# Optimization experiments

Hardware: AMD Instinct MI355X
Metric: run time of the kernel (lower is better)

Reference implementation:

```python
import jax, jax.numpy as jnp
import numpy as np
import math

DIM = 2048; H = 16; QR = 1536; KVR = 512; DN = 128; DR = 64; DV = 128
BS = 4; S = 1024
QK_HEAD = DN + DR  # 192


def _rms(x, w, eps=1e-6):
    v = jnp.mean(x * x, axis=-1, keepdims=True)
    return w * (x * jax.lax.rsqrt(v + eps))


def _rope_cos_sin(seq_len, dim):
    inv_freq = 1.0 / (10000.0 ** (jnp.arange(0, dim, 2, dtype=jnp.float32) / dim))
    t = jnp.arange(seq_len, dtype=jnp.float32)
    freqs = jnp.einsum('s,d->sd', t, inv_freq)
    freqs = jnp.concatenate([freqs, freqs], axis=-1)  # [S, dim]
    return jnp.cos(freqs), jnp.sin(freqs)


def _rotate_half(x):
    x1, x2 = jnp.split(x, 2, axis=-1)
    return jnp.concatenate([-x2, x1], axis=-1)


def setup_inputs() -> dict:
    key = jax.random.key(0)
    ks = jax.random.split(key, 12)
    sd = 0.02
    x = jax.random.normal(ks[0], (BS, S, DIM), dtype=jnp.float32)
    # causal additive mask [b, s, t]
    i = jnp.arange(S)
    causal = jnp.where(i[:, None] >= i[None, :], 0.0, -1e9).astype(jnp.float32)
    mask = jnp.broadcast_to(causal, (BS, S, S))
    return {
        'x': x,
        'mask': mask,
        'wq_a_w': jax.random.normal(ks[1], (QR, DIM)) * sd,
        'wq_a_b': jnp.zeros((QR,), jnp.float32),
        'q_norm_w': jnp.ones((QR,), jnp.float32),
        'wq_b_w': jax.random.normal(ks[2], (H * QK_HEAD, QR)) * sd,
        'wq_b_b': jnp.zeros((H * QK_HEAD,), jnp.float32),
        'wkv_a_w': jax.random.normal(ks[3], (KVR + DR, DIM)) * sd,
        'wkv_a_b': jnp.zeros((KVR + DR,), jnp.float32),
        'kv_norm_w': jnp.ones((KVR,), jnp.float32),
        'wkv_b_w': jax.random.normal(ks[4], (H * (DN + DV), KVR)) * sd,
        'wo_w': jax.random.normal(ks[5], (DIM, H * DV)) * sd,
        'wo_b': jnp.zeros((DIM,), jnp.float32),
    }


def reference(x, mask, wq_a_w, wq_a_b, q_norm_w, wq_b_w, wq_b_b,
              wkv_a_w, wkv_a_b, kv_norm_w, wkv_b_w, wo_w, wo_b):
    bs, seq_len, _ = x.shape
    # Q low-rank path
    q = x @ wq_a_w.T + wq_a_b                     # [b,s,QR]
    q = _rms(q, q_norm_w)
    q = q @ wq_b_w.T + wq_b_b                     # [b,s,H*192]
    q = q.reshape(bs, seq_len, H, QK_HEAD)
    q_nope, q_pe = q[..., :DN], q[..., DN:]       # [b,s,h,128], [b,s,h,64]
    # compressed KV path
    kv = x @ wkv_a_w.T + wkv_a_b                  # [b,s,KVR+64]
    c, k_pe = kv[..., :KVR], kv[..., KVR:]        # [b,s,512], [b,s,64]
    # RoPE on the rope sub-dims
    cos, sin = _rope_cos_sin(seq_len, DR)         # [s,64]
    cos4 = cos[None, :, None, :]
    sin4 = sin[None, :, None, :]
    q_pe = q_pe * cos4 + _rotate_half(q_pe) * sin4
    k_pe4 = k_pe[:, :, None, :]
    k_pe = (k_pe4 * cos4 + _rotate_half(k_pe4) * sin4)[:, :, 0, :]  # [b,s,64]
    # weight absorption: wkv_b viewed [H, DN+DV, KVR]
    wkv_b = wkv_b_w.reshape(H, DN + DV, KVR)
    q_abs = jnp.einsum('bshd,hdc->bshc', q_nope, wkv_b[:, :DN])      # [b,s,h,512]
    c_n = _rms(c, kv_norm_w)                                         # [b,t,512]
    scores = (jnp.einsum('bshc,btc->bsht', q_abs, c_n)
              + jnp.einsum('bshr,btr->bsht', q_pe, k_pe)) / math.sqrt(QK_HEAD)
    scores = scores + mask[:, :, None, :]
    scores = jax.nn.softmax(scores, axis=-1)
    o = jnp.einsum('bsht,btc->bshc', scores, c_n)                    # [b,s,h,512]
    o = jnp.einsum('bshc,hdc->bshd', o, wkv_b[:, -DV:])              # [b,s,h,128]
    o = o.reshape(bs, seq_len, H * DV)
    return o @ wo_w.T + wo_b
```

## Files before the change

### kernel.cpp

```cpp
#include <hip/hip_runtime.h>


typedef __attribute__((ext_vector_type(8))) short bf16x8;
typedef __attribute__((ext_vector_type(4))) float f32x4;
typedef __attribute__((ext_vector_type(4))) int i32x4;
typedef unsigned short ushort_t;
typedef unsigned int uint32;

typedef const __attribute__((address_space(1))) void* gas_ptr;
typedef __attribute__((address_space(3))) void* las_ptr;

#define DEV __device__ __forceinline__
#define WAITVM(N) asm volatile("s_waitcnt vmcnt(" #N ")" ::: "memory")
#define WAITLGKM0 asm volatile("s_waitcnt lgkmcnt(0)" ::: "memory")

DEV float b2f(ushort_t u) { return __uint_as_float(((uint32)u) << 16); }
DEV ushort_t f2b(float f) {
  uint32 u = __float_as_uint(f);
  return (ushort_t)((u + 0x7fffu + ((u >> 16) & 1u)) >> 16);
}
DEV uint32 pkb(float lo, float hi) { return (uint32)f2b(lo) | ((uint32)f2b(hi) << 16); }

DEV void c4seg(const float4* __restrict__ in, ushort4* __restrict__ out, int i, int n4) {
  if (i < n4) {
    float4 v = in[i];
    ushort4 o; o.x = f2b(v.x); o.y = f2b(v.y); o.z = f2b(v.z); o.w = f2b(v.w);
    out[i] = o;
  }
}
DEV void vbseg(const float* __restrict__ in, ushort_t* __restrict__ out, int i4, int dofs) {
  int c4 = i4 & 127, d = (i4 >> 7) & 127, h = i4 >> 14;
  const float4 v = *(const float4*)(in + ((long)(h * 256 + dofs + d)) * 512 + c4 * 4);
  ushort4 o; o.x = f2b(v.x); o.y = f2b(v.y); o.z = f2b(v.z); o.w = f2b(v.w);
  ((ushort4*)out)[i4] = o;
}
__global__ __launch_bounds__(256) void castall_k(
    const float* __restrict__ x, const float* __restrict__ wq_a_w,
    const float* __restrict__ wkv_a_w, const float* __restrict__ wq_b_w,
    const float* __restrict__ wo_w, const float* __restrict__ wkv_b_w,
    ushort_t* __restrict__ xb, ushort_t* __restrict__ wcomb,
    ushort_t* __restrict__ wqb, ushort_t* __restrict__ wo,
    ushort_t* __restrict__ wkvbv, ushort_t* __restrict__ wkvbn) {
  int blk = blockIdx.x, tid = threadIdx.x;
  if (blk < 8192) {
    c4seg((const float4*)x, (ushort4*)xb, blk * 256 + tid, 2097152);
  } else if (blk < 11264) {
    c4seg((const float4*)wq_a_w, (ushort4*)wcomb, (blk - 8192) * 256 + tid, 786432);
  } else if (blk < 12416) {
    c4seg((const float4*)wkv_a_w, (ushort4*)(wcomb + 1536 * 2048),
          (blk - 11264) * 256 + tid, 294912);
  } else if (blk < 17024) {
    c4seg((const float4*)wq_b_w, (ushort4*)wqb, (blk - 12416) * 256 + tid, 1179648);
  } else if (blk < 21120) {
    c4seg((const float4*)wo_w, (ushort4*)wo, (blk - 17024) * 256 + tid, 1048576);
  } else if (blk < 22144) {
    vbseg(wkv_b_w, wkvbv, (blk - 21120) * 256 + tid, 128);
  } else {
    vbseg(wkv_b_w, wkvbn, (blk - 22144) * 256 + tid, 0);
  }
}

__global__ __launch_bounds__(512) void rmskv_k(const float* __restrict__ qa_in,
                                               ushort_t* __restrict__ qan,
                                               const float* __restrict__ q_norm_w,
                                               const float* __restrict__ kvf,
                                               const float* __restrict__ kv_norm_w,
                                               ushort_t* __restrict__ kcat,
                                               ushort_t* __restrict__ vtp,
                                               ushort_t* __restrict__ kabs) {
  __shared__ float sbuf[8];
  __shared__ ushort_t sh[8 * 512];
  int blk = blockIdx.x, tid = threadIdx.x;
  int wv = tid >> 6, lane = tid & 63;
  if (blk < 4096) {
    long row = blk;
    const float* p = qa_in + row * 1536;
    float v0 = p[tid], v1 = p[tid + 512], v2 = p[tid + 1024];
    float ss = v0 * v0 + v1 * v1 + v2 * v2;
#pragma unroll
    for (int d = 1; d <= 32; d <<= 1) ss += __shfl_xor(ss, d);
    if (lane == 0) sbuf[wv] = ss;
    __syncthreads();
    float tot = 0.f;
#pragma unroll
    for (int i = 0; i < 8; ++i) tot += sbuf[i];
    float sc = rsqrtf(tot * (1.0f / 1536.0f) + 1e-6f);
    qan[row * 1536 + tid] = f2b(v0 * sc * q_norm_w[tid]);
    qan[row * 1536 + tid + 512] = f2b(v1 * sc * q_norm_w[tid + 512]);
    qan[row * 1536 + tid + 1024] = f2b(v2 * sc * q_norm_w[tid + 1024]);
  } else {
    int kb = blk - 4096;
    long row = (long)kb * 8 + wv;
    const float* p = kvf + row * 576;
    float4 v0 = *(const float4*)(p + lane * 8);
    float4 v1 = *(const float4*)(p + lane * 8 + 4);
    float ss = v0.x * v0.x + v0.y * v0.y + v0.z * v0.z + v0.w * v0.w
             + v1.x * v1.x + v1.y * v1.y + v1.z * v1.z + v1.w * v1.w;
#pragma unroll
    for (int d = 1; d <= 32; d <<= 1) ss += __shfl_xor(ss, d);
    float sc = rsqrtf(ss * (1.0f / 512.0f) + 1e-6f);
    float4 w0 = *(const float4*)(kv_norm_w + lane * 8);
    float4 w1 = *(const float4*)(kv_norm_w + lane * 8 + 4);
    ushort_t tmp[8];
    tmp[0] = f2b(v0.x * sc * w0.x); tmp[1] = f2b(v0.y * sc * w0.y);
    tmp[2] = f2b(v0.z * sc * w0.z); tmp[3] = f2b(v0.w * sc * w0.w);
    tmp[4] = f2b(v1.x * sc * w1.x); tmp[5] = f2b(v1.y * sc * w1.y);
    tmp[6] = f2b(v1.z * sc * w1.z); tmp[7] = f2b(v1.w * sc * w1.w);
    *(uint4*)(kcat + row * 576 + lane * 8) = *(uint4*)tmp;
    *(uint4*)(sh + wv * 512 + lane * 8) = *(uint4*)tmp;
    if (lane < 32) {
      int t = (int)(row & 1023);
      float x1 = p[512 + lane], x2 = p[544 + lane];
      float ang = (float)t * powf(10000.0f, -(float)lane * (1.0f / 32.0f));
      float s, c; sincosf(ang, &s, &c);
      ushort_t r1 = f2b(x1 * c - x2 * s), r2 = f2b(x2 * c + x1 * s);
      kcat[row * 576 + 512 + lane] = r1;
      kcat[row * 576 + 544 + lane] = r2;
#pragma unroll
      for (int h = 0; h < 16; ++h) {
        long base = ((long)h * 4096 + row) * 192;
        kabs[base + 128 + lane] = r1;
        kabs[base + 160 + lane] = r2;
      }
    }
    __syncthreads();
    ushort_t t8[8];
#pragma unroll
    for (int j = 0; j < 8; ++j) t8[j] = sh[j * 512 + tid];
    int b = kb >> 7, tb = kb & 127;
    *(uint4*)(vtp + (((long)b * 128 + tb) * 512 + tid) * 8) = *(uint4*)t8;
  }
}

template <bool OUT_BF16>
__global__ __launch_bounds__(256) void gemm_bt_k(
    const ushort_t* __restrict__ A, int lda, long sAz,
    const ushort_t* __restrict__ B, int ldb, long sBz,
    void* __restrict__ C, int ldc, long sCz,
    const float* __restrict__ bias, float scale,
    int M, int N, int K) {
  __shared__ ushort_t As[2 * 4096];
  __shared__ ushort_t Bs[2 * 4096];
  int tid = threadIdx.x;
  int wave = tid >> 6, lane = tid & 63;
  int row0 = blockIdx.x * 128, col0 = blockIdx.y * 128;
  int z = blockIdx.z;
  const ushort_t* Az = A + (long)z * sAz;
  const ushort_t* Bz = B + (long)z * sBz;
  int wr = wave >> 1, wc = wave & 1;
  int lr = lane & 15, kq = lane >> 4;

  f32x4 acc[4][4];
#pragma unroll
  for (int m = 0; m < 4; ++m)
#pragma unroll
    for (int n = 0; n < 4; ++n) acc[m][n] = (f32x4){0.f, 0.f, 0.f, 0.f};

  auto stage = [&](int buf, int k0) {
#pragma unroll
    for (int rnd = 0; rnd < 2; ++rnd) {
      int e = rnd * 2048 + wave * 512 + lane * 8;
      int tr = e >> 5, tc = e & 31;
      int ar = row0 + tr; if (ar >= M) ar = M - 1;
      int br = col0 + tr; if (br >= N) br = N - 1;
      __builtin_amdgcn_global_load_lds((gas_ptr)(Az + (long)ar * lda + (k0 + tc)),
          (las_ptr)(As + buf * 4096 + rnd * 2048 + wave * 512), 16, 0, 0);
      __builtin_amdgcn_global_load_lds((gas_ptr)(Bz + (long)br * ldb + (k0 + tc)),
          (las_ptr)(Bs + buf * 4096 + rnd * 2048 + wave * 512), 16, 0, 0);
    }
  };

  stage(0, 0);
  int nk = K >> 5;
  for (int kt = 0; kt < nk; ++kt) {
    int cur = kt & 1;
    if (kt + 1 < nk) { stage(cur ^ 1, (kt + 1) * 32); WAITVM(4); }
    else { WAITVM(0); }
    __builtin_amdgcn_s_barrier();
    __builtin_amdgcn_sched_barrier(0);
    const ushort_t* Ac = As + cur * 4096;
    const ushort_t* Bc = Bs + cur * 4096;
    bf16x8 a[4], bb[4];
#pragma unroll
    for (int m = 0; m < 4; ++m)
      a[m] = *(const bf16x8*)(Ac + (wr * 64 + m * 16 + lr) * 32 + kq * 8);
#pragma unroll
    for (int n = 0; n < 4; ++n)
      bb[n] = *(const bf16x8*)(Bc + (wc * 64 + n * 16 + lr) * 32 + kq * 8);
#pragma unroll
    for (int m = 0; m < 4; ++m)
#pragma unroll
      for (int n = 0; n < 4; ++n)
        acc[m][n] = __builtin_amdgcn_mfma_f32_16x16x32_bf16(bb[n], a[m], acc[m][n], 0, 0, 0);
    __builtin_amdgcn_s_barrier();
  }

#pragma unroll
  for (int m = 0; m < 4; ++m) {
    int gr = row0 + wr * 64 + m * 16 + lr;
    if (gr >= M) continue;
#pragma unroll
    for (int n = 0; n < 4; ++n) {
      int cb = col0 + wc * 64 + n * 16 + kq * 4;
      if (cb >= N) continue;
      f32x4 v = acc[m][n];
#pragma unroll
      for (int r = 0; r < 4; ++r) v[r] = v[r] * scale + (bias ? bias[cb + r] : 0.f);
      long ci = (long)z * sCz + (long)gr * ldc + cb;
      if constexpr (OUT_BF16) {
        ushort4 pk; pk.x = f2b(v[0]); pk.y = f2b(v[1]); pk.z = f2b(v[2]); pk.w = f2b(v[3]);
        *(ushort4*)((ushort_t*)C + ci) = pk;
      } else {
        *(f32x4*)((float*)C + ci) = v;
      }
    }
  }
}

template <int MODE>
__global__ __launch_bounds__(256) void gemm64_k(
    const ushort_t* __restrict__ A, int lda,
    const ushort_t* __restrict__ B, int ldb,
    void* __restrict__ C, int ldc,
    const float* __restrict__ bias,
    void* __restrict__ C2, const float* __restrict__ bias2,
    int M, int N, int K) {
  __shared__ ushort_t As[2 * 8192];
  __shared__ ushort_t Bs[2 * 8192];
  int tid = threadIdx.x;
  int wave = tid >> 6, lane = tid & 63;
  int bid = blockIdx.y * gridDim.x + blockIdx.x;
  int nwg = gridDim.x * gridDim.y;
  int swz = (bid & 7) * (nwg >> 3) + (bid >> 3);
  int bx = swz % gridDim.x, by = swz / gridDim.x;
  int row0 = bx * 128, col0 = by * 128;
  int wr = wave >> 1, wc = wave & 1;
  int lr = lane & 15, kq = lane >> 4;
  int rsw = lr & 7;

  f32x4 acc[4][4];
#pragma unroll
  for (int m = 0; m < 4; ++m)
#pragma unroll
    for (int n = 0; n < 4; ++n) acc[m][n] = (f32x4){0.f, 0.f, 0.f, 0.f};

  auto stage = [&](int buf, int k0) {
#pragma unroll
    for (int ii = 0; ii < 4; ++ii) {
      int e = ii * 256 + tid;
      int r = e >> 3, c = e & 7;
      int scol = ((c ^ (r & 7)) << 3);
      int ar = row0 + r; if (ar >= M) ar = M - 1;
      int br = col0 + r; if (br >= N) br = N - 1;
      __builtin_amdgcn_global_load_lds((gas_ptr)(A + (long)ar * lda + k0 + scol),
          (las_ptr)(As + buf * 8192 + e * 8), 16, 0, 0);
      __builtin_amdgcn_global_load_lds((gas_ptr)(B + (long)br * ldb + k0 + scol),
          (las_ptr)(Bs + buf * 8192 + e * 8), 16, 0, 0);
    }
  };

  stage(0, 0);
  int nk = K >> 6;
  for (int kt = 0; kt < nk; ++kt) {
    int cur = kt & 1;
    if (kt + 1 < nk) { stage(cur ^ 1, (kt + 1) * 64); WAITVM(8); }
    else { WAITVM(0); }
    __builtin_amdgcn_s_barrier();
    __builtin_amdgcn_sched_barrier(0);
    const ushort_t* Ac = As + cur * 8192;
    const ushort_t* Bc = Bs + cur * 8192;
#pragma unroll
    for (int ks = 0; ks < 2; ++ks) {
      bf16x8 a[4], bb[4];
#pragma unroll
      for (int m = 0; m < 4; ++m) {
        int row = wr * 64 + m * 16 + lr;
        a[m] = *(const bf16x8*)(Ac + row * 64 + ((((ks << 2) | kq) ^ rsw) << 3));
      }
#pragma unroll
      for (int n = 0; n < 4; ++n) {
        int row = wc * 64 + n * 16 + lr;
        bb[n] = *(const bf16x8*)(Bc + row * 64 + ((((ks << 2) | kq) ^ rsw) << 3));
      }
#pragma unroll
      for (int m = 0; m < 4; ++m)
#pragma unroll
        for (int n = 0; n < 4; ++n)
          acc[m][n] = __builtin_amdgcn_mfma_f32_16x16x32_bf16(bb[n], a[m], acc[m][n], 0, 0, 0);
    }
    __builtin_amdgcn_s_barrier();
  }

  if constexpr (MODE == 0) {
#pragma unroll
    for (int m = 0; m < 4; ++m) {
      int gr = row0 + wr * 64 + m * 16 + lr;
      if (gr >= M) continue;
#pragma unroll
      for (int n = 0; n < 4; ++n) {
        int cb = col0 + wc * 64 + n * 16 + kq * 4;
        if (cb >= N) continue;
        f32x4 v = acc[m][n];
#pragma unroll
        for (int r = 0; r < 4; ++r) v[r] += bias[cb + r];
        *(f32x4*)((float*)C + (long)gr * ldc + cb) = v;
      }
    }
  } else if constexpr (MODE == 1) {
#pragma unroll
    for (int m = 0; m < 4; ++m) {
      int gr = row0 + wr * 64 + m * 16 + lr;
      if (gr >= M) continue;
#pragma unroll
      for (int n = 0; n < 4; ++n) {
        int cb = col0 + wc * 64 + n * 16 + kq * 4;
        if (cb >= N) continue;
        f32x4 v = acc[m][n];
        if (cb < 1536) {
#pragma unroll
          for (int r = 0; r < 4; ++r) v[r] += bias[cb + r];
          *(f32x4*)((float*)C + (long)gr * 1536 + cb) = v;
        } else {
          int c2 = cb - 1536;
#pragma unroll
          for (int r = 0; r < 4; ++r) v[r] += bias2[c2 + r];
          *(f32x4*)((float*)C2 + (long)gr * 576 + c2) = v;
        }
      }
    }
  } else {
    const float RS = 0.07216878364870322f;
#pragma unroll
    for (int n = 0; n < 4; ++n) {
      int cb = col0 + wc * 64 + n * 16 + kq * 4;
      int h = cb / 192, d0 = cb - h * 192;
      ushort_t* qh = (ushort_t*)C + (long)h * 4096 * 192;
      if (d0 < 128) {
        f32x4 bv;
#pragma unroll
        for (int r = 0; r < 4; ++r) bv[r] = bias[cb + r];
#pragma unroll
        for (int m = 0; m < 4; ++m) {
          int gr = row0 + wr * 64 + m * 16 + lr;
          f32x4 v = acc[m][n];
          ushort4 pk;
          pk.x = f2b((v[0] + bv[0]) * RS); pk.y = f2b((v[1] + bv[1]) * RS);
          pk.z = f2b((v[2] + bv[2]) * RS); pk.w = f2b((v[3] + bv[3]) * RS);
          *(ushort4*)(qh + (long)gr * 192 + d0) = pk;
        }
      } else if (d0 < 160) {
        int nn = (n < 2) ? n : 0;
        f32x4 bv1, bv2, invf;
#pragma unroll
        for (int r = 0; r < 4; ++r) {
          bv1[r] = bias[cb + r]; bv2[r] = bias[cb + 32 + r];
          invf[r] = powf(10000.0f, -(float)(d0 - 128 + r) * (1.0f / 32.0f));
        }
#pragma unroll
        for (int m = 0; m < 4; ++m) {
          int gr = row0 + wr * 64 + m * 16 + lr;
          int t = gr & 1023;
          f32x4 v1 = acc[m][nn], v2 = acc[m][nn + 2];
          ushort4 p1, p2;
#pragma unroll
          for (int r = 0; r < 4; ++r) {
            float s, c; sincosf((float)t * invf[r], &s, &c);
            float x1 = v1[r] + bv1[r], x2 = v2[r] + bv2[r];
            ((ushort_t*)&p1)[r] = f2b((x1 * c - x2 * s) * RS);
            ((ushort_t*)&p2)[r] = f2b((x2 * c + x1 * s) * RS);
          }
          *(ushort4*)(qh + (long)gr * 192 + d0) = p1;
          *(ushort4*)(qh + (long)gr * 192 + d0 + 32) = p2;
        }
      }
    }
  }
}

__global__ __launch_bounds__(512, 1) void flash7_k(const ushort_t* __restrict__ qcat2,
                                                   const ushort_t* __restrict__ kabs,
                                                   const ushort_t* __restrict__ vtp,
                                                   ushort_t* __restrict__ O) {
  __shared__ __align__(16) ushort_t SMEM[6400 + 2 * 16384];

  int tid = threadIdx.x;
  int wave = tid >> 6, lane = tid & 63;
  int lr = lane & 15, kq = lane >> 4;
  int bi = blockIdx.x;
  int jz = bi >> 6;
  int qb = (jz < 4) ? jz : 11 - jz;
  int bh = bi & 63;
  int h = bh >> 2, b = bh & 3;
  int s0 = qb * 128;
  int nt = (qb + 1) * 4;

  const ushort_t* kt = kabs + ((long)h * 4096 + b * 1024) * 192;
  const ushort_t* vt = vtp + (long)b * 524288;
  const ushort_t* qp = qcat2 + ((long)(h * 4096 + b * 1024 + s0 + wave * 16 + lr)) * 192 + kq * 8;

  auto stageK = [&](int t0) {
    const ushort_t* sb = kt + (long)t0 * 192;
#pragma unroll
    for (int ii = 0; ii < 2; ++ii) {
      int c = ii * 512 + tid;
      if (ii == 1 && tid >= 288) break;
      int t = (int)((unsigned)c / 25u);
      int r = c - t * 25;
      int rr = (r == 24) ? 0 : r;
      const ushort_t* src = sb + t * 192 + rr * 8;
      __builtin_amdgcn_global_load_lds((gas_ptr)src, (las_ptr)(SMEM + c * 8), 16, 0, 0);
    }
  };
  auto stageV = [&](int buf, int t0) {
    const ushort_t* sb = vt + (long)(t0 >> 3) * 4096;
    ushort_t* vb = SMEM + 6400 + buf * 16384;
#pragma unroll
    for (int ii = 0; ii < 4; ++ii) {
      int c0 = (ii * 8 + wave) * 64;
      const ushort_t* src = sb + (long)(c0 + lane) * 8;
      __builtin_amdgcn_global_load_lds((gas_ptr)src, (las_ptr)(vb + c0 * 8), 16, 0, 0);
    }
  };

  stageK(0); stageV(0, 0);
  bf16x8 qreg[6];
#pragma unroll
  for (int st = 0; st < 6; ++st) qreg[st] = *(const bf16x8*)(qp + st * 32);

  f32x4 o[32];
#pragma unroll
  for (int v = 0; v < 32; ++v) o[v] = (f32x4){0.f, 0.f, 0.f, 0.f};
  float m_run = -1e30f, l_run = 0.f;

  int row_g = s0 + wave * 16 + lr;
  int idx_lo = (((kq & 1) << 5) + lr) << 2;
  int idx_hi = idx_lo + 64;
  bool losel = (kq < 2);

  __syncthreads();

  for (int it = 0; it < nt; ++it) {
    int cur = it & 1;
    f32x4 sv0 = (f32x4){0.f, 0.f, 0.f, 0.f}, sv1 = sv0;
    __builtin_amdgcn_s_setprio(1);
#pragma unroll
    for (int st = 0; st < 6; ++st) {
      int off = st * 32 + kq * 8;
      bf16x8 k0 = *(const bf16x8*)(SMEM + lr * 200 + off);
      bf16x8 k1 = *(const bf16x8*)(SMEM + (16 + lr) * 200 + off);
      sv0 = __builtin_amdgcn_mfma_f32_16x16x32_bf16(k0, qreg[st], sv0, 0, 0, 0);
      sv1 = __builtin_amdgcn_mfma_f32_16x16x32_bf16(k1, qreg[st], sv1, 0, 0, 0);
    }
    __builtin_amdgcn_s_setprio(0);
    WAITLGKM0;
    __builtin_amdgcn_sched_barrier(0);
    __builtin_amdgcn_s_barrier();
    if (it + 1 < nt) { stageK((it + 1) * 32); stageV(cur ^ 1, (it + 1) * 32); }
    int t0 = it * 32;
    if (t0 >= s0) {
#pragma unroll
      for (int rr = 0; rr < 4; ++rr) {
        if (t0 + kq * 4 + rr > row_g) sv0[rr] = -1e30f;
        if (t0 + 16 + kq * 4 + rr > row_g) sv1[rr] = -1e30f;
      }
    }
    float mx = fmaxf(fmaxf(fmaxf(sv0[0], sv0[1]), fmaxf(sv0[2], sv0[3])),
                     fmaxf(fmaxf(sv1[0], sv1[1]), fmaxf(sv1[2], sv1[3])));
    mx = fmaxf(mx, __shfl_xor(mx, 16));
    mx = fmaxf(mx, __shfl_xor(mx, 32));
    float mn = (mx > m_run + 8.0f) ? mx : m_run;
    float alpha = __expf(m_run - mn);
    float p0 = __expf(sv0[0] - mn), p1 = __expf(sv0[1] - mn);
    float p2 = __expf(sv0[2] - mn), p3 = __expf(sv0[3] - mn);
    float p4 = __expf(sv1[0] - mn), p5 = __expf(sv1[1] - mn);
    float p6 = __expf(sv1[2] - mn), p7 = __expf(sv1[3] - mn);
    float psum = ((p0 + p1) + (p2 + p3)) + ((p4 + p5) + (p6 + p7));
    psum += __shfl_xor(psum, 16);
    psum += __shfl_xor(psum, 32);
    l_run = l_run * alpha + psum;
    m_run = mn;
    int u0 = (int)pkb(p0, p1), u1 = (int)pkb(p2, p3);
    int u2 = (int)pkb(p4, p5), u3 = (int)pkb(p6, p7);
    int b00 = __builtin_amdgcn_ds_bpermute(idx_lo, u0);
    int b10 = __builtin_amdgcn_ds_bpermute(idx_lo, u1);
    int b20 = __builtin_amdgcn_ds_bpermute(idx_lo, u2);
    int b30 = __builtin_amdgcn_ds_bpermute(idx_lo, u3);
    int b01 = __builtin_amdgcn_ds_bpermute(idx_hi, u0);
    int b11 = __builtin_amdgcn_ds_bpermute(idx_hi, u1);
    int b21 = __builtin_amdgcn_ds_bpermute(idx_hi, u2);
    int b31 = __builtin_amdgcn_ds_bpermute(idx_hi, u3);
    i32x4 w;
    w.x = losel ? b00 : b20; w.y = losel ? b10 : b30;
    w.z = losel ? b01 : b21; w.w = losel ? b11 : b31;
    bf16x8 pa = __builtin_bit_cast(bf16x8, w);
    float a0 = __shfl(alpha, kq * 4 + 0), a1 = __shfl(alpha, kq * 4 + 1);
    float a2 = __shfl(alpha, kq * 4 + 2), a3 = __shfl(alpha, kq * 4 + 3);
    if (__any((a0 != 1.f) | (a1 != 1.f) | (a2 != 1.f) | (a3 != 1.f))) {
      f32x4 av; av[0] = a0; av[1] = a1; av[2] = a2; av[3] = a3;
#pragma unroll
      for (int v = 0; v < 32; ++v) o[v] *= av;
    }
    const ushort_t* Vc = SMEM + 6400 + cur * 16384 + (kq * 512 + lr) * 8;
    __builtin_amdgcn_s_setprio(1);
#pragma unroll
    for (int v = 0; v < 32; ++v) {
      bf16x8 bv = *(const bf16x8*)(Vc + v * 128);
      o[v] = __builtin_amdgcn_mfma_f32_16x16x32_bf16(pa, bv, o[v], 0, 0, 0);
    }
    __builtin_amdgcn_s_setprio(0);
    WAITVM(0);
    __builtin_amdgcn_s_barrier();
  }
  float l0 = __shfl(l_run, kq * 4 + 0), l1 = __shfl(l_run, kq * 4 + 1);
  float l2 = __shfl(l_run, kq * 4 + 2), l3 = __shfl(l_run, kq * 4 + 3);
  f32x4 inv; inv[0] = 1.f / l0; inv[1] = 1.f / l1; inv[2] = 1.f / l2; inv[3] = 1.f / l3;
  ushort_t* ob = O + ((long)(h * 4096 + b * 1024 + s0 + wave * 16 + kq * 4)) * 512 + lr;
#pragma unroll
  for (int rr = 0; rr < 4; ++rr) {
    ushort_t* orow = ob + (long)rr * 512;
#pragma unroll
    for (int v = 0; v < 32; ++v) orow[v * 16] = f2b(o[v][rr] * inv[rr]);
  }
}

extern "C" void kernel_launch(void* const* d_in, const int* in_sizes, int n_in,
                              void* d_out, int out_size, void* d_ws, size_t ws_size,
                              hipStream_t stream) {
  (void)in_sizes; (void)n_in;
  const float* x         = (const float*)d_in[0];
  const float* wq_a_w    = (const float*)d_in[2];
  const float* wq_a_b    = (const float*)d_in[3];
  const float* q_norm_w  = (const float*)d_in[4];
  const float* wq_b_w    = (const float*)d_in[5];
  const float* wq_b_b    = (const float*)d_in[6];
  const float* wkv_a_w   = (const float*)d_in[7];
  const float* wkv_a_b   = (const float*)d_in[8];
  const float* kv_norm_w = (const float*)d_in[9];
  const float* wkv_b_w   = (const float*)d_in[10];
  const float* wo_w      = (const float*)d_in[11];
  const float* wo_b      = (const float*)d_in[12];

  char* ws = (char*)d_ws;
  constexpr size_t OFF_XB     = 0;
  constexpr size_t OFF_WCOMB  = 16777216;
  constexpr size_t OFF_WQB    = 25427968;
  constexpr size_t OFF_QA     = 34865152;
  constexpr size_t OFF_QAN    = 60030976;
  constexpr size_t OFF_QCAT2  = 72613888;
  constexpr size_t OFF_WKVBN  = 97779712;
  constexpr size_t OFF_WKVBV  = 99876864;
  constexpr size_t OFF_WO     = 101974016;
  constexpr size_t OFF_KVF    = 110362624;
  constexpr size_t OFF_KCAT   = 119799808;
  constexpr size_t OFF_VTP    = 124518400;
  constexpr size_t OFF_KABS   = 128712704;
  constexpr size_t OFF_O      = 153878528;
  constexpr size_t OFF_O2     = 220987392;
  constexpr size_t WS_NEED    = 237764608;
  if (ws_size < WS_NEED) {
    (void)hipMemsetAsync(d_out, 0, (size_t)out_size * sizeof(float), stream);
    return;
  }

  ushort_t* xb     = (ushort_t*)(ws + OFF_XB);
  ushort_t* wcomb  = (ushort_t*)(ws + OFF_WCOMB);
  ushort_t* wqb    = (ushort_t*)(ws + OFF_WQB);
  float*    qa     = (float*)(ws + OFF_QA);
  ushort_t* qan    = (ushort_t*)(ws + OFF_QAN);
  ushort_t* qcat2  = (ushort_t*)(ws + OFF_QCAT2);
  ushort_t* wkvbn  = (ushort_t*)(ws + OFF_WKVBN);
  ushort_t* wkvbv  = (ushort_t*)(ws + OFF_WKVBV);
  ushort_t* wo     = (ushort_t*)(ws + OFF_WO);
  float*    kvf    = (float*)(ws + OFF_KVF);
  ushort_t* kcat   = (ushort_t*)(ws + OFF_KCAT);
  ushort_t* vtp    = (ushort_t*)(ws + OFF_VTP);
  ushort_t* kabs   = (ushort_t*)(ws + OFF_KABS);
  ushort_t* Obuf   = (ushort_t*)(ws + OFF_O);
  ushort_t* o2     = (ushort_t*)(ws + OFF_O2);

  castall_k<<<23168, 256, 0, stream>>>(x, wq_a_w, wkv_a_w, wq_b_w, wo_w, wkv_b_w,
                                       xb, wcomb, wqb, wo, wkvbv, wkvbn);
  gemm64_k<1><<<dim3(32, 17), 256, 0, stream>>>(xb, 2048, wcomb, 2048,
      qa, 1536, wq_a_b, kvf, wkv_a_b, 4096, 2112, 2048);
  rmskv_k<<<4608, 512, 0, stream>>>(qa, qan, q_norm_w, kvf, kv_norm_w, kcat, vtp, kabs);
  gemm64_k<2><<<dim3(32, 24), 256, 0, stream>>>(qan, 1536, wqb, 1536,
      qcat2, 0, wq_b_b, nullptr, nullptr, 4096, 3072, 1536);
  gemm_bt_k<true><<<dim3(32, 1, 16), 256, 0, stream>>>(kcat, 576, 0,
      wkvbn, 512, (long)128 * 512, kabs, 192, (long)4096 * 192,
      nullptr, 1.f, 4096, 128, 512);
  flash7_k<<<512, 512, 0, stream>>>(qcat2, kabs, vtp, Obuf);
  gemm_bt_k<true><<<dim3(32, 1, 16), 256, 0, stream>>>(Obuf, 512, (long)4096 * 512,
      wkvbv, 512, (long)128 * 512, o2, 2048, 128, nullptr, 1.f, 4096, 128, 512);
  gemm64_k<0><<<dim3(32, 16), 256, 0, stream>>>(o2, 2048, wo, 2048,
      (float*)d_out, 2048, wo_b, nullptr, nullptr, 4096, 2048, 2048);
}
```

Before: 384.9 us.

## Double-buffer K tiles in flash kernel and stage GEMM epilogue through LDS

The flash attention kernel now double-buffers the K tile as well as V, so the next K/V loads are issued at the top of each iteration. This removes the mid-iteration barrier that previously waited for the K reads to finish before prefetching, leaving a single __syncthreads per tile. Separately, the fp32 GEMM epilogue (modes 0/1) writes accumulators into shared memory and then stores full contiguous rows, aiming for coalesced global writes in exchange for extra LDS traffic and barriers. Doubling the K buffer raises the flash kernel's LDS footprint.

Result: faster. 354.0 us (-8.0%).

```diff
diff --git a/kernel.cpp b/kernel.cpp
--- a/kernel.cpp
+++ b/kernel.cpp
@@ -12,7 +12,6 @@
 
 #define DEV __device__ __forceinline__
 #define WAITVM(N) asm volatile("s_waitcnt vmcnt(" #N ")" ::: "memory")
-#define WAITLGKM0 asm volatile("s_waitcnt lgkmcnt(0)" ::: "memory")
 
 DEV float b2f(ushort_t u) { return __uint_as_float(((uint32)u) << 16); }
 DEV ushort_t f2b(float f) {
@@ -225,8 +224,9 @@
     const float* __restrict__ bias,
     void* __restrict__ C2, const float* __restrict__ bias2,
     int M, int N, int K) {
-  __shared__ ushort_t As[2 * 8192];
-  __shared__ ushort_t Bs[2 * 8192];
+  __shared__ ushort_t SM[32768];
+  ushort_t* As = SM;
+  ushort_t* Bs = SM + 16384;
   int tid = threadIdx.x;
   int wave = tid >> 6, lane = tid & 63;
   int bid = blockIdx.y * gridDim.x + blockIdx.x;
@@ -291,42 +291,51 @@
     __builtin_amdgcn_s_barrier();
   }
 
-  if constexpr (MODE == 0) {
-#pragma unroll
-    for (int m = 0; m < 4; ++m) {
-      int gr = row0 + wr * 64 + m * 16 + lr;
-      if (gr >= M) continue;
-#pragma unroll
-      for (int n = 0; n < 4; ++n) {
-        int cb = col0 + wc * 64 + n * 16 + kq * 4;
-        if (cb >= N) continue;
-        f32x4 v = acc[m][n];
-#pragma unroll
-        for (int r = 0; r < 4; ++r) v[r] += bias[cb + r];
-        *(f32x4*)((float*)C + (long)gr * ldc + cb) = v;
-      }
-    }
-  } else if constexpr (MODE == 1) {
-#pragma unroll
-    for (int m = 0; m < 4; ++m) {
-      int gr = row0 + wr * 64 + m * 16 + lr;
-      if (gr >= M) continue;
-#pragma unroll
-      for (int n = 0; n < 4; ++n) {
-        int cb = col0 + wc * 64 + n * 16 + kq * 4;
-        if (cb >= N) continue;
-        f32x4 v = acc[m][n];
-        if (cb < 1536) {
-#pragma unroll
-          for (int r = 0; r < 4; ++r) v[r] += bias[cb + r];
-          *(f32x4*)((float*)C + (long)gr * 1536 + cb) = v;
-        } else {
-          int c2 = cb - 1536;
-#pragma unroll
-          for (int r = 0; r < 4; ++r) v[r] += bias2[c2 + r];
-          *(f32x4*)((float*)C2 + (long)gr * 576 + c2) = v;
+  if constexpr (MODE == 0 || MODE == 1) {
+    float* fs = (float*)SM;
+#pragma unroll
+    for (int p = 0; p < 2; ++p) {
+      if (wr == p) {
+#pragma unroll
+        for (int m = 0; m < 4; ++m) {
+#pragma unroll
+          for (int n = 0; n < 4; ++n) {
+            int rl = m * 16 + lr;
+            int cl = wc * 64 + n * 16 + kq * 4;
+            int cb = col0 + cl;
+            int cbb = (cb + 3 < N) ? cb : (N - 4);
+            f32x4 v = acc[m][n];
+#pragma unroll
+            for (int r = 0; r < 4; ++r) {
+              float bv;
+              if constexpr (MODE == 1)
+                bv = (cbb + r < 1536) ? bias[cbb + r] : bias2[cbb + r - 1536];
+              else
+                bv = bias[cbb + r];
+              v[r] += bv;
+            }
+            *(f32x4*)&fs[rl * 132 + cl] = v;
+          }
         }
       }
+      __syncthreads();
+#pragma unroll
+      for (int j = 0; j < 8; ++j) {
+        int u = j * 256 + tid;
+        int rl = u >> 5, off = (u & 31) << 2;
+        int gr = row0 + p * 64 + rl;
+        int gc = col0 + off;
+        if (gr < M && gc < N) {
+          f32x4 vv = *(const f32x4*)&fs[rl * 132 + off];
+          if constexpr (MODE == 1) {
+            if (gc < 1536) *(f32x4*)((float*)C + (long)gr * 1536 + gc) = vv;
+            else           *(f32x4*)((float*)C2 + (long)gr * 576 + (gc - 1536)) = vv;
+          } else {
+            *(f32x4*)((float*)C + (long)gr * ldc + gc) = vv;
+          }
+        }
+      }
+      __syncthreads();
     }
   } else {
     const float RS = 0.07216878364870322f;
@@ -377,11 +386,11 @@
   }
 }
 
-__global__ __launch_bounds__(512, 1) void flash7_k(const ushort_t* __restrict__ qcat2,
+__global__ __launch_bounds__(512, 1) void flash5_k(const ushort_t* __restrict__ qcat2,
                                                    const ushort_t* __restrict__ kabs,
                                                    const ushort_t* __restrict__ vtp,
                                                    ushort_t* __restrict__ O) {
-  __shared__ __align__(16) ushort_t SMEM[6400 + 2 * 16384];
+  __shared__ __align__(16) ushort_t SMEM[2 * 6400 + 2 * 16384];
 
   int tid = threadIdx.x;
   int wave = tid >> 6, lane = tid & 63;
@@ -398,8 +407,9 @@
   const ushort_t* vt = vtp + (long)b * 524288;
   const ushort_t* qp = qcat2 + ((long)(h * 4096 + b * 1024 + s0 + wave * 16 + lr)) * 192 + kq * 8;
 
-  auto stageK = [&](int t0) {
+  auto stageK = [&](int buf, int t0) {
     const ushort_t* sb = kt + (long)t0 * 192;
+    ushort_t* kb = SMEM + buf * 6400;
 #pragma unroll
     for (int ii = 0; ii < 2; ++ii) {
       int c = ii * 512 + tid;
@@ -408,12 +418,12 @@
       int r = c - t * 25;
       int rr = (r == 24) ? 0 : r;
       const ushort_t* src = sb + t * 192 + rr * 8;
-      __builtin_amdgcn_global_load_lds((gas_ptr)src, (las_ptr)(SMEM + c * 8), 16, 0, 0);
+      __builtin_amdgcn_global_load_lds((gas_ptr)src, (las_ptr)(kb + c * 8), 16, 0, 0);
     }
   };
   auto stageV = [&](int buf, int t0) {
     const ushort_t* sb = vt + (long)(t0 >> 3) * 4096;
-    ushort_t* vb = SMEM + 6400 + buf * 16384;
+    ushort_t* vb = SMEM + 12800 + buf * 16384;
 #pragma unroll
     for (int ii = 0; ii < 4; ++ii) {
       int c0 = (ii * 8 + wave) * 64;
@@ -422,7 +432,7 @@
     }
   };
 
-  stageK(0); stageV(0, 0);
+  stageK(0, 0); stageV(0, 0);
   bf16x8 qreg[6];
 #pragma unroll
   for (int st = 0; st < 6; ++st) qreg[st] = *(const bf16x8*)(qp + st * 32);
@@ -441,21 +451,19 @@
 
   for (int it = 0; it < nt; ++it) {
     int cur = it & 1;
+    if (it + 1 < nt) { stageK(cur ^ 1, (it + 1) * 32); stageV(cur ^ 1, (it + 1) * 32); }
+    const ushort_t* Kc = SMEM + cur * 6400;
     f32x4 sv0 = (f32x4){0.f, 0.f, 0.f, 0.f}, sv1 = sv0;
     __builtin_amdgcn_s_setprio(1);
 #pragma unroll
     for (int st = 0; st < 6; ++st) {
       int off = st * 32 + kq * 8;
-      bf16x8 k0 = *(const bf16x8*)(SMEM + lr * 200 + off);
-      bf16x8 k1 = *(const bf16x8*)(SMEM + (16 + lr) * 200 + off);
+      bf16x8 k0 = *(const bf16x8*)(Kc + lr * 200 + off);
+      bf16x8 k1 = *(const bf16x8*)(Kc + (16 + lr) * 200 + off);
       sv0 = __builtin_amdgcn_mfma_f32_16x16x32_bf16(k0, qreg[st], sv0, 0, 0, 0);
       sv1 = __builtin_amdgcn_mfma_f32_16x16x32_bf16(k1, qreg[st], sv1, 0, 0, 0);
     }
     __builtin_amdgcn_s_setprio(0);
-    WAITLGKM0;
-    __builtin_amdgcn_sched_barrier(0);
-    __builtin_amdgcn_s_barrier();
-    if (it + 1 < nt) { stageK((it + 1) * 32); stageV(cur ^ 1, (it + 1) * 32); }
     int t0 = it * 32;
     if (t0 >= s0) {
 #pragma unroll
@@ -500,7 +508,7 @@
 #pragma unroll
       for (int v = 0; v < 32; ++v) o[v] *= av;
     }
-    const ushort_t* Vc = SMEM + 6400 + cur * 16384 + (kq * 512 + lr) * 8;
+    const ushort_t* Vc = SMEM + 12800 + cur * 16384 + (kq * 512 + lr) * 8;
     __builtin_amdgcn_s_setprio(1);
 #pragma unroll
     for (int v = 0; v < 32; ++v) {
@@ -508,8 +516,7 @@
       o[v] = __builtin_amdgcn_mfma_f32_16x16x32_bf16(pa, bv, o[v], 0, 0, 0);
     }
     __builtin_amdgcn_s_setprio(0);
-    WAITVM(0);
-    __builtin_amdgcn_s_barrier();
+    __syncthreads();
   }
   float l0 = __shfl(l_run, kq * 4 + 0), l1 = __shfl(l_run, kq * 4 + 1);
   float l2 = __shfl(l_run, kq * 4 + 2), l3 = __shfl(l_run, kq * 4 + 3);
@@ -588,7 +595,7 @@
   gemm_bt_k<true><<<dim3(32, 1, 16), 256, 0, stream>>>(kcat, 576, 0,
       wkvbn, 512, (long)128 * 512, kabs, 192, (long)4096 * 192,
       nullptr, 1.f, 4096, 128, 512);
-  flash7_k<<<512, 512, 0, stream>>>(qcat2, kabs, vtp, Obuf);
+  flash5_k<<<512, 512, 0, stream>>>(qcat2, kabs, vtp, Obuf);
   gemm_bt_k<true><<<dim3(32, 1, 16), 256, 0, stream>>>(Obuf, 512, (long)4096 * 512,
       wkvbv, 512, (long)128 * 512, o2, 2048, 128, nullptr, 1.f, 4096, 128, 512);
   gemm64_k<0><<<dim3(32, 16), 256, 0, stream>>>(o2, 2048, wo, 2048,
```
